# Optimization experiments

Hardware: AMD Instinct MI355X
Metric: run time of the kernel (lower is better)

## Reference

```python
import jax, jax.numpy as jnp
from jax import lax
import numpy as np

INPUT = 42
HIDDEN = 64
OUT = 2


def setup_inputs() -> dict:
    key = jax.random.key(0)
    ks = jax.random.split(key, 7)
    T, B = 2048, 512
    s_ih = 1.0 / np.sqrt(HIDDEN)
    return {
        "x": jax.random.normal(ks[0], (T, B, INPUT), dtype=jnp.float32),
        "W_ih": jax.random.uniform(ks[1], (4 * HIDDEN, INPUT), jnp.float32, -s_ih, s_ih),
        "W_hh": jax.random.uniform(ks[2], (4 * HIDDEN, HIDDEN), jnp.float32, -s_ih, s_ih),
        "b_ih": jax.random.uniform(ks[3], (4 * HIDDEN,), jnp.float32, -s_ih, s_ih),
        "b_hh": jax.random.uniform(ks[4], (4 * HIDDEN,), jnp.float32, -s_ih, s_ih),
        "W_out": jax.random.uniform(ks[5], (OUT, HIDDEN), jnp.float32, -s_ih, s_ih),
        "b_out": jax.random.uniform(ks[6], (OUT,), jnp.float32, -s_ih, s_ih),
    }


def reference(x, W_ih, W_hh, b_ih, b_hh, W_out, b_out):
    # x: (T, B, 42); PyTorch LSTM gate order: i, f, g, o
    B = x.shape[1]
    h0 = jnp.zeros((B, HIDDEN), x.dtype)
    c0 = jnp.zeros((B, HIDDEN), x.dtype)
    # Precompute input projections for all timesteps in one GEMM.
    x_proj = jnp.einsum('tbi,gi->tbg', x, W_ih) + b_ih + b_hh  # (T, B, 4H)

    def step(carry, xp):
        h, c = carry
        gates = xp + h @ W_hh.T  # (B, 4H)
        i, f, g, o = jnp.split(gates, 4, axis=-1)
        c = jax.nn.sigmoid(f) * c + jax.nn.sigmoid(i) * jnp.tanh(g)
        h = jax.nn.sigmoid(o) * jnp.tanh(c)
        return (h, c), h

    _, lstm_out = lax.scan(step, (h0, c0), x_proj)  # (T, B, H)
    # Faithful to original: lstm_out[:, -1, :] -> last BATCH element, all timesteps
    return lstm_out[:, -1, :] @ W_out.T + b_out  # (T, 2)
```

## Files before the change

kernel.cpp:

```cpp
#include <hip/hip_runtime.h>
#include <hip/hip_bf16.h>


#define T_STEPS 2048
#define BATCH   512
#define NIN     42
#define NH      64
#define NG      256
#define CH      8
#define NCHUNK  (T_STEPS / CH)
#define XT      16

#define LOG2E 1.44269504f

#if __has_builtin(__builtin_amdgcn_exp2f)
#define EXP2F __builtin_amdgcn_exp2f
#else
#define EXP2F exp2f
#endif

typedef float v2f __attribute__((ext_vector_type(2)));

__global__ __launch_bounds__(256) void xproj_kernel(
    const float* __restrict__ x, const float* __restrict__ W_ih,
    const float* __restrict__ b_ih, const float* __restrict__ b_hh,
    float* __restrict__ xp)
{
    const int g  = threadIdx.x;
    const int t0 = blockIdx.x * XT;
    __shared__ float ws[NG * NIN];
    __shared__ float xs[XT][NIN];
    for (int i = threadIdx.x; i < NG * NIN; i += 256) ws[i] = W_ih[i];
    for (int i = threadIdx.x; i < XT * NIN; i += 256) {
        int tt = i / NIN, j = i % NIN;
        xs[tt][j] = x[((size_t)(t0 + tt) * BATCH + (BATCH - 1)) * NIN + j];
    }
    const float bias = b_ih[g] + b_hh[g];
    __syncthreads();
    const float* wr = &ws[g * NIN];
    for (int tt = 0; tt < XT; ++tt) {
        float s = bias;
#pragma unroll
        for (int i = 0; i < NIN; ++i) s += wr[i] * xs[tt][i];
        xp[(size_t)(t0 + tt) * NG + g] = s * LOG2E;
    }
}

__device__ __forceinline__ void wg_barrier_lgkm() {
    asm volatile("s_waitcnt lgkmcnt(0)\n\ts_barrier" ::: "memory");
}

__device__ __forceinline__ void pin2(v2f& v) {
    asm volatile("" : "+v"(v));
}

template <int CTRL>
__device__ __forceinline__ float dpp_xadd(float v) {
    int s = __builtin_amdgcn_mov_dpp(__float_as_int(v), CTRL, 0xF, 0xF, true);
    return v + __int_as_float(s);
}

__device__ __forceinline__ float sigmoid2(float xs) {
    return __builtin_amdgcn_rcpf(1.f + EXP2F(-xs));
}
__device__ __forceinline__ float tanh2(float xs) {
    return __builtin_fmaf(-2.f,
        __builtin_amdgcn_rcpf(1.f + EXP2F(xs + xs)), 1.f);
}
__device__ __forceinline__ float tanhc(float c) {
    return __builtin_fmaf(-2.f,
        __builtin_amdgcn_rcpf(1.f + EXP2F(c * (2.f * LOG2E))), 1.f);
}

__device__ __forceinline__ v2f fma2(v2f a, v2f b, v2f c) {
    return __builtin_elementwise_fma(a, b, c);
}

__global__ void
__attribute__((amdgpu_flat_work_group_size(256, 256), amdgpu_waves_per_eu(1, 1)))
lstm_scan_kernel(
    const float* __restrict__ W_hh, const float* __restrict__ xp,
    float* __restrict__ hout)
{
    const int lane = threadIdx.x;
    const int kc   = lane & 3;
    const int u    = lane >> 2;

    __shared__ __align__(16) float hbuf[2][NH];
    if (lane < NH) { hbuf[0][lane] = 0.f; hbuf[1][lane] = 0.f; }

    const v2f* W0 = (const v2f*)(W_hh + (0 * NH + u) * NH + kc * 16);
    const v2f* W1 = (const v2f*)(W_hh + (1 * NH + u) * NH + kc * 16);
    const v2f* W2 = (const v2f*)(W_hh + (2 * NH + u) * NH + kc * 16);
    const v2f* W3 = (const v2f*)(W_hh + (3 * NH + u) * NH + kc * 16);
    const v2f SC = {LOG2E, LOG2E};
    v2f w0a=W0[0]*SC, w0b=W0[1]*SC, w0c=W0[2]*SC, w0d=W0[3]*SC,
        w0e=W0[4]*SC, w0f=W0[5]*SC, w0g=W0[6]*SC, w0h=W0[7]*SC;
    v2f w1a=W1[0]*SC, w1b=W1[1]*SC, w1c=W1[2]*SC, w1d=W1[3]*SC,
        w1e=W1[4]*SC, w1f=W1[5]*SC, w1g=W1[6]*SC, w1h=W1[7]*SC;
    v2f w2a=W2[0]*SC, w2b=W2[1]*SC, w2c=W2[2]*SC, w2d=W2[3]*SC,
        w2e=W2[4]*SC, w2f=W2[5]*SC, w2g=W2[6]*SC, w2h=W2[7]*SC;
    v2f w3a=W3[0]*SC, w3b=W3[1]*SC, w3c=W3[2]*SC, w3d=W3[3]*SC,
        w3e=W3[4]*SC, w3f=W3[5]*SC, w3g=W3[6]*SC, w3h=W3[7]*SC;
    pin2(w0a); pin2(w0b); pin2(w0c); pin2(w0d); pin2(w0e); pin2(w0f); pin2(w0g); pin2(w0h);
    pin2(w1a); pin2(w1b); pin2(w1c); pin2(w1d); pin2(w1e); pin2(w1f); pin2(w1g); pin2(w1h);
    pin2(w2a); pin2(w2b); pin2(w2c); pin2(w2d); pin2(w2e); pin2(w2f); pin2(w2g); pin2(w2h);
    pin2(w3a); pin2(w3b); pin2(w3c); pin2(w3d); pin2(w3e); pin2(w3f); pin2(w3g); pin2(w3h);

    float c = 0.f;
    const int seed_off = kc * NH + u;
    float* __restrict__ hp = hout + u;

    float xq[CH];
#pragma unroll
    for (int tt = 0; tt < CH; ++tt) xq[tt] = xp[tt * NG + seed_off];

    wg_barrier_lgkm();

    for (int ch = 0; ch < NCHUNK; ++ch) {
        float xn[CH];
        if (ch + 1 < NCHUNK) {
#pragma unroll
            for (int tt = 0; tt < CH; ++tt)
                xn[tt] = xp[(size_t)(ch + 1) * (CH * NG) + tt * NG + seed_off];
        }

#pragma unroll
        for (int tt = 0; tt < CH; ++tt) {
            const int p = tt & 1;
            const float4* hb = (const float4*)hbuf[p];
            float4 hv0 = hb[kc * 4 + 0];
            float4 hv1 = hb[kc * 4 + 1];
            float4 hv2 = hb[kc * 4 + 2];
            float4 hv3 = hb[kc * 4 + 3];
            v2f h0 = {hv0.x, hv0.y}, h1 = {hv0.z, hv0.w};
            v2f h2 = {hv1.x, hv1.y}, h3 = {hv1.z, hv1.w};
            v2f h4 = {hv2.x, hv2.y}, h5 = {hv2.z, hv2.w};
            v2f h6 = {hv3.x, hv3.y}, h7 = {hv3.z, hv3.w};

            v2f a0 = {(kc == 0) ? xq[tt] : 0.f, 0.f};
            v2f a1 = {(kc == 1) ? xq[tt] : 0.f, 0.f};
            v2f a2 = {(kc == 2) ? xq[tt] : 0.f, 0.f};
            v2f a3 = {(kc == 3) ? xq[tt] : 0.f, 0.f};

            a0 = fma2(w0a, h0, a0); a0 = fma2(w0b, h1, a0);
            a0 = fma2(w0c, h2, a0); a0 = fma2(w0d, h3, a0);
            a0 = fma2(w0e, h4, a0); a0 = fma2(w0f, h5, a0);
            a0 = fma2(w0g, h6, a0); a0 = fma2(w0h, h7, a0);
            a1 = fma2(w1a, h0, a1); a1 = fma2(w1b, h1, a1);
            a1 = fma2(w1c, h2, a1); a1 = fma2(w1d, h3, a1);
            a1 = fma2(w1e, h4, a1); a1 = fma2(w1f, h5, a1);
            a1 = fma2(w1g, h6, a1); a1 = fma2(w1h, h7, a1);
            a2 = fma2(w2a, h0, a2); a2 = fma2(w2b, h1, a2);
            a2 = fma2(w2c, h2, a2); a2 = fma2(w2d, h3, a2);
            a2 = fma2(w2e, h4, a2); a2 = fma2(w2f, h5, a2);
            a2 = fma2(w2g, h6, a2); a2 = fma2(w2h, h7, a2);
            a3 = fma2(w3a, h0, a3); a3 = fma2(w3b, h1, a3);
            a3 = fma2(w3c, h2, a3); a3 = fma2(w3d, h3, a3);
            a3 = fma2(w3e, h4, a3); a3 = fma2(w3f, h5, a3);
            a3 = fma2(w3g, h6, a3); a3 = fma2(w3h, h7, a3);

            float s0 = a0.x + a0.y;
            float s1 = a1.x + a1.y;
            float s2 = a2.x + a2.y;
            float s3 = a3.x + a3.y;

            s0 = dpp_xadd<0xB1>(s0); s1 = dpp_xadd<0xB1>(s1);
            s2 = dpp_xadd<0xB1>(s2); s3 = dpp_xadd<0xB1>(s3);
            s0 = dpp_xadd<0x4E>(s0); s1 = dpp_xadd<0x4E>(s1);
            s2 = dpp_xadd<0x4E>(s2); s3 = dpp_xadd<0x4E>(s3);

            float i_ = sigmoid2(s0);
            float f_ = sigmoid2(s1);
            float g_ = tanh2(s2);
            float o_ = sigmoid2(s3);

            c = f_ * c + i_ * g_;
            float hn = o_ * tanhc(c);

            if (kc == 0) {
                hbuf[1 - p][u] = hn;
                hp[(size_t)(ch * CH + tt) * NH] = hn;
            }
            wg_barrier_lgkm();
        }

#pragma unroll
        for (int tt = 0; tt < CH; ++tt) xq[tt] = xn[tt];
    }
}

__global__ __launch_bounds__(256) void outproj_kernel(
    const float* __restrict__ hout, const float* __restrict__ W_out,
    const float* __restrict__ b_out, float* __restrict__ out)
{
    int idx = blockIdx.x * blockDim.x + threadIdx.x;
    if (idx >= T_STEPS * 2) return;
    int t = idx >> 1, o = idx & 1;
    const float* hr = hout + (size_t)t * NH;
    const float* wr = W_out + o * NH;
    float s = b_out[o];
#pragma unroll
    for (int j = 0; j < NH; ++j) s += hr[j] * wr[j];
    out[t * 2 + o] = s;
}

extern "C" void kernel_launch(void* const* d_in, const int* in_sizes, int n_in,
                              void* d_out, int out_size, void* d_ws, size_t ws_size,
                              hipStream_t stream) {
    const float* x     = (const float*)d_in[0];
    const float* W_ih  = (const float*)d_in[1];
    const float* W_hh  = (const float*)d_in[2];
    const float* b_ih  = (const float*)d_in[3];
    const float* b_hh  = (const float*)d_in[4];
    const float* W_out = (const float*)d_in[5];
    const float* b_out = (const float*)d_in[6];
    float* out = (float*)d_out;

    float* xp   = (float*)d_ws;
    float* hout = xp + (size_t)T_STEPS * NG;

    xproj_kernel<<<T_STEPS / XT, 256, 0, stream>>>(x, W_ih, b_ih, b_hh, xp);
    lstm_scan_kernel<<<1, 256, 0, stream>>>(W_hh, xp, hout);
    outproj_kernel<<<(T_STEPS * 2 + 255) / 256, 256, 0, stream>>>(hout, W_out, b_out, out);
}
```

Before: 839.4 us.

## Distribute gate reductions and activations across the quad lanes via DPP transpose

Replaces the four-way butterfly all-reduce, in which every lane of a quad reduced and activated all four gates, with a transpose-style reduce. Each lane now ends up owning one gate's sum and computes a single sigmoid or tanh through a unified exp/rcp formula with per-lane coefficients. The gate values are then exchanged with DPP moves to form the cell and hidden update. This cuts the redundant transcendental and add work on the serial per-step critical path, at the cost of extra selects and DPP moves. The input projection is also folded into the exponent FMA instead of seeding the accumulator.

```diff
diff --git a/kernel.cpp b/kernel.cpp
--- a/kernel.cpp
+++ b/kernel.cpp
@@ -55,21 +55,9 @@
 }
 
 template <int CTRL>
-__device__ __forceinline__ float dpp_xadd(float v) {
-    int s = __builtin_amdgcn_mov_dpp(__float_as_int(v), CTRL, 0xF, 0xF, true);
-    return v + __int_as_float(s);
-}
-
-__device__ __forceinline__ float sigmoid2(float xs) {
-    return __builtin_amdgcn_rcpf(1.f + EXP2F(-xs));
-}
-__device__ __forceinline__ float tanh2(float xs) {
-    return __builtin_fmaf(-2.f,
-        __builtin_amdgcn_rcpf(1.f + EXP2F(xs + xs)), 1.f);
-}
-__device__ __forceinline__ float tanhc(float c) {
-    return __builtin_fmaf(-2.f,
-        __builtin_amdgcn_rcpf(1.f + EXP2F(c * (2.f * LOG2E))), 1.f);
+__device__ __forceinline__ float dpp_mov(float v) {
+    return __int_as_float(
+        __builtin_amdgcn_mov_dpp(__float_as_int(v), CTRL, 0xF, 0xF, true));
 }
 
 __device__ __forceinline__ v2f fma2(v2f a, v2f b, v2f c) {
@@ -88,6 +76,13 @@
 
     __shared__ __align__(16) float hbuf[2][NH];
     if (lane < NH) { hbuf[0][lane] = 0.f; hbuf[1][lane] = 0.f; }
+
+    const bool istanh = (kc == 2);
+    const float gm = istanh ?  2.f : -1.f;
+    const float gA = istanh ? -2.f :  1.f;
+    const float gB = istanh ?  1.f :  0.f;
+    const bool lo = (kc & 1) != 0;
+    const bool hi = (kc & 2) != 0;
 
     const v2f* W0 = (const v2f*)(W_hh + (0 * NH + u) * NH + kc * 16);
     const v2f* W1 = (const v2f*)(W_hh + (1 * NH + u) * NH + kc * 16);
@@ -111,9 +106,9 @@
     const int seed_off = kc * NH + u;
     float* __restrict__ hp = hout + u;
 
-    float xq[CH];
-#pragma unroll
-    for (int tt = 0; tt < CH; ++tt) xq[tt] = xp[tt * NG + seed_off];
+    float mxq[CH];
+#pragma unroll
+    for (int tt = 0; tt < CH; ++tt) mxq[tt] = gm * xp[tt * NG + seed_off];
 
     wg_barrier_lgkm();
 
@@ -138,10 +133,7 @@
             v2f h4 = {hv2.x, hv2.y}, h5 = {hv2.z, hv2.w};
             v2f h6 = {hv3.x, hv3.y}, h7 = {hv3.z, hv3.w};
 
-            v2f a0 = {(kc == 0) ? xq[tt] : 0.f, 0.f};
-            v2f a1 = {(kc == 1) ? xq[tt] : 0.f, 0.f};
-            v2f a2 = {(kc == 2) ? xq[tt] : 0.f, 0.f};
-            v2f a3 = {(kc == 3) ? xq[tt] : 0.f, 0.f};
+            v2f a0 = {0.f, 0.f}, a1 = {0.f, 0.f}, a2 = {0.f, 0.f}, a3 = {0.f, 0.f};
 
             a0 = fma2(w0a, h0, a0); a0 = fma2(w0b, h1, a0);
             a0 = fma2(w0c, h2, a0); a0 = fma2(w0d, h3, a0);
@@ -160,23 +152,35 @@
             a3 = fma2(w3e, h4, a3); a3 = fma2(w3f, h5, a3);
             a3 = fma2(w3g, h6, a3); a3 = fma2(w3h, h7, a3);
 
-            float s0 = a0.x + a0.y;
-            float s1 = a1.x + a1.y;
-            float s2 = a2.x + a2.y;
-            float s3 = a3.x + a3.y;
-
-            s0 = dpp_xadd<0xB1>(s0); s1 = dpp_xadd<0xB1>(s1);
-            s2 = dpp_xadd<0xB1>(s2); s3 = dpp_xadd<0xB1>(s3);
-            s0 = dpp_xadd<0x4E>(s0); s1 = dpp_xadd<0x4E>(s1);
-            s2 = dpp_xadd<0x4E>(s2); s3 = dpp_xadd<0x4E>(s3);
-
-            float i_ = sigmoid2(s0);
-            float f_ = sigmoid2(s1);
-            float g_ = tanh2(s2);
-            float o_ = sigmoid2(s3);
-
-            c = f_ * c + i_ * g_;
-            float hn = o_ * tanhc(c);
+            float p0 = a0.x + a0.y;
+            float p1 = a1.x + a1.y;
+            float p2 = a2.x + a2.y;
+            float p3 = a3.x + a3.y;
+
+            float k01 = lo ? p1 : p0;
+            float s01 = lo ? p0 : p1;
+            float k23 = lo ? p3 : p2;
+            float s23 = lo ? p2 : p3;
+            float r0 = k01 + dpp_mov<0xB1>(s01);
+            float r1 = k23 + dpp_mov<0xB1>(s23);
+            float kf = hi ? r1 : r0;
+            float sf = hi ? r0 : r1;
+            float s  = kf + dpp_mov<0x4E>(sf);
+
+            float e = EXP2F(__builtin_fmaf(gm, s, mxq[tt]));
+            float r = __builtin_amdgcn_rcpf(1.f + e);
+            float v = __builtin_fmaf(gA, r, gB);
+
+            float w  = dpp_mov<0xB1>(v);
+            float g0 = dpp_mov<0x4E>(v);
+            float oo = dpp_mov<0x4E>(w);
+
+            float t   = v * g0;
+            float p2o = -2.f * oo;
+            c = __builtin_fmaf(w, c, t);
+            float e2 = EXP2F(c * (2.f * LOG2E));
+            float rr = __builtin_amdgcn_rcpf(1.f + e2);
+            float hn = __builtin_fmaf(p2o, rr, oo);
 
             if (kc == 0) {
                 hbuf[1 - p][u] = hn;
@@ -186,7 +190,7 @@
         }
 
 #pragma unroll
-        for (int tt = 0; tt < CH; ++tt) xq[tt] = xn[tt];
+        for (int tt = 0; tt < CH; ++tt) mxq[tt] = gm * xn[tt];
     }
 }
 
```

Result: faster. 758.6 us (-9.6%).
